# Kernel tuning notes

Measured on AMD Instinct MI355X. Metric: run time of the kernel, lower is better.

Reference implementation:

```python
import jax, jax.numpy as jnp
import numpy as np

NUM_HEADS = 16

def setup_inputs() -> dict:
    key = jax.random.key(0)
    k1, k2, k3 = jax.random.split(key, 3)
    B, S, D = 4, 2048, 1024
    x = jax.random.normal(k1, (B, S, D), dtype=jnp.float32)
    # xavier-uniform-like small init so unscaled logits stay numerically sane
    w_qkv = jax.random.normal(k2, (3 * D, D), dtype=jnp.float32) * 0.02
    w_out = jax.random.normal(k3, (D, D), dtype=jnp.float32) * 0.02
    return {"x": x, "w_qkv": w_qkv, "w_out": w_out}

def reference(x, w_qkv, w_out):
    B, S, D = x.shape
    H = NUM_HEADS
    d = D // H
    # qkv projection (Linear, no bias): x @ W^T -> [B, S, 3D]
    qkv = jnp.einsum('bsd,ed->bse', x, w_qkv).reshape(B, S, H, 3 * d)
    q, k, v = jnp.split(qkv, 3, axis=-1)           # each [B, S, H, d]
    q = q.transpose(0, 2, 1, 3)                    # [B, H, S, d]
    k = k.transpose(0, 2, 1, 3)
    v = v.transpose(0, 2, 1, 3)
    # NOTE: the original module does NOT scale by 1/sqrt(d) — faithful.
    logits = jnp.einsum('bhqd,bhkd->bhqk', q, k)   # [B, H, S, S]
    attn = jax.nn.softmax(logits, axis=-1)
    vals = jnp.einsum('bhqk,bhkd->bhqd', attn, v)  # [B, H, S, d]
    vals = vals.transpose(0, 2, 1, 3).reshape(B, S, D)
    return jnp.einsum('bsd,od->bso', vals, w_out)
```

## Files before the change

kernel.cpp:

```cpp
#include <hip/hip_runtime.h>
#include <hip/hip_bf16.h>

#define DEVINL __device__ __forceinline__

typedef short bf16x4 __attribute__((ext_vector_type(4)));
typedef short bf16x8 __attribute__((ext_vector_type(8)));
typedef float f32x4 __attribute__((ext_vector_type(4)));
typedef float f32x16 __attribute__((ext_vector_type(16)));
typedef unsigned short us4 __attribute__((ext_vector_type(4)));


DEVINL unsigned short f2bf(float f) {
  unsigned u = __builtin_bit_cast(unsigned, f);
  unsigned r = u + 0x7fffu + ((u >> 16) & 1u);
  return (unsigned short)(r >> 16);
}

DEVINL f32x4 mfma32(bf16x8 a, bf16x8 b, f32x4 c) {
  return __builtin_amdgcn_mfma_f32_16x16x32_bf16(a, b, c, 0, 0, 0);
}

DEVINL f32x16 mfma3216(bf16x8 a, bf16x8 b, f32x16 c) {
  return __builtin_amdgcn_mfma_f32_32x32x16_bf16(a, b, c, 0, 0, 0);
}

DEVINL float fexp2(float x) {
#if __has_builtin(__builtin_amdgcn_exp2f)
  return __builtin_amdgcn_exp2f(x);
#else
  return exp2f(x);
#endif
}

DEVINL unsigned cvt_pk_bf16(float a, float b) {
  unsigned r;
  asm("v_cvt_pk_bf16_f32 %0, %1, %2" : "=v"(r) : "v"(a), "v"(b));
  return r;
}

DEVINL void permswap(unsigned& x, unsigned& y) {
#if __has_builtin(__builtin_amdgcn_permlane32_swap)
  typedef int i32x2_t __attribute__((ext_vector_type(2)));
  i32x2_t r = __builtin_amdgcn_permlane32_swap((int)x, (int)y, false, false);
  x = (unsigned)r[0];
  y = (unsigned)r[1];
#else
  asm("v_permlane32_swap_b32 %0, %1" : "+v"(x), "+v"(y));
#endif
}

#define GLOAD_LDS16(g, l)                                                    \
  __builtin_amdgcn_global_load_lds(                                          \
      (__attribute__((address_space(1))) void*)(unsigned short*)(g),         \
      (__attribute__((address_space(3))) void*)(l), 16, 0, 0)

__global__ void cvtk(const float* __restrict__ src,
                     unsigned short* __restrict__ dst, int n4) {
  int i = blockIdx.x * 256 + threadIdx.x;
  const int st = gridDim.x * 256;
  for (; i < n4; i += st) {
    const float4 v = ((const float4*)src)[i];
    us4 o;
    o[0] = f2bf(v.x); o[1] = f2bf(v.y); o[2] = f2bf(v.z); o[3] = f2bf(v.w);
    ((us4*)dst)[i] = o;
  }
}

__global__ __launch_bounds__(256, 2) void qkv_gemm(
    const unsigned short* __restrict__ A,
    const unsigned short* __restrict__ Bw,
    unsigned short* __restrict__ Qo,
    unsigned short* __restrict__ Ko,
    unsigned short* __restrict__ VTo) {
  constexpr int K = 1024;
  __shared__ unsigned short SH[16384];
  const int tid = threadIdx.x;
  const int lane = tid & 63;
  const int wid = tid >> 6;
  const int l15 = lane & 15, g = lane >> 4;
  const int fid = blockIdx.y * 24 + blockIdx.x;
  const int swzid = (fid & 7) * 192 + (fid >> 3);
  const int m0 = (swzid / 24) * 128;
  const int n0 = (swzid % 24) * 128;
  const int wr = wid >> 1, wc = wid & 1;

  f32x4 acc[4][4] = {};

  const int sidx0 = tid * 8;
  const int sidx1 = (256 + tid) * 8;
  const int r0 = sidx0 >> 5, c0 = sidx0 & 31;
  const int r1 = sidx1 >> 5, c1 = sidx1 & 31;

#define QSTAGE(kt, bb)                                                       \
  {                                                                          \
    const int k0_ = (kt)*32;                                                 \
    GLOAD_LDS16(A + (size_t)(m0 + r0) * K + k0_ + c0,                        \
                SH + (bb)*8192 + sidx0);                                     \
    GLOAD_LDS16(Bw + (size_t)(n0 + r0) * K + k0_ + c0,                       \
                SH + (bb)*8192 + 4096 + sidx0);                              \
    GLOAD_LDS16(A + (size_t)(m0 + r1) * K + k0_ + c1,                        \
                SH + (bb)*8192 + sidx1);                                     \
    GLOAD_LDS16(Bw + (size_t)(n0 + r1) * K + k0_ + c1,                       \
                SH + (bb)*8192 + 4096 + sidx1);                              \
  }

  QSTAGE(0, 0);
  __syncthreads();

  for (int t = 0; t < 32; ++t) {
    const int cb = t & 1;
    if (t < 31) QSTAGE(t + 1, cb ^ 1);
    bf16x8 af[4], bfr[4];
#pragma unroll
    for (int i = 0; i < 4; ++i) {
      af[i] =
          *(const bf16x8*)(SH + cb * 8192 + (wr * 64 + i * 16 + l15) * 32 +
                           g * 8);
      bfr[i] = *(const bf16x8*)(SH + cb * 8192 + 4096 +
                                (wc * 64 + i * 16 + l15) * 32 + g * 8);
    }
#pragma unroll
    for (int mi = 0; mi < 4; ++mi)
#pragma unroll
      for (int ni = 0; ni < 4; ++ni)
        acc[mi][ni] = mfma32(af[mi], bfr[ni], acc[mi][ni]);
    __syncthreads();
  }
#undef QSTAGE

#pragma unroll
  for (int ni = 0; ni < 4; ++ni) {
    const int ebase = n0 + wc * 64 + ni * 16;
    const int h = ebase / 192;
    const int rbase = ebase - h * 192;
#pragma unroll
    for (int mi = 0; mi < 4; ++mi) {
      const int mbase = m0 + wr * 64 + mi * 16 + g * 4;
      if (rbase >= 128) {
        const int rv = rbase + l15 - 128;
        const int b = mbase >> 11, s = mbase & 2047;
        const int bh = b * 16 + h;
        us4 ov;
#pragma unroll
        for (int j = 0; j < 4; ++j) ov[j] = f2bf(acc[mi][ni][j]);
        *(us4*)(VTo + ((size_t)bh * 64 + rv) * 2048 + s) = ov;
      } else {
        const float scale = (rbase < 64) ? 1.44269504f : 1.0f;
        const int eloc = wc * 64 + ni * 16 + l15;
        const int mloc = wr * 64 + mi * 16 + g * 4;
#pragma unroll
        for (int j = 0; j < 4; ++j)
          SH[(mloc + j) * 128 + eloc] = f2bf(acc[mi][ni][j] * scale);
      }
    }
  }
  __syncthreads();
#pragma unroll
  for (int k = 0; k < 8; ++k) {
    const int c = tid + k * 256;
    const int ml = c >> 4, e8 = (c & 15) * 8;
    const int e0 = n0 + e8;
    const int h = e0 / 192;
    const int r = e0 - h * 192;
    if (r < 128) {
      const int mm = m0 + ml;
      const int b = mm >> 11, s = mm & 2047;
      const int bh = b * 16 + h;
      const bf16x8 v = *(const bf16x8*)&SH[ml * 128 + e8];
      if (r < 64)
        *(bf16x8*)(Qo + ((size_t)bh * 2048 + s) * 64 + r) = v;
      else
        *(bf16x8*)(Ko + ((size_t)bh * 2048 + s) * 64 + (r - 64)) = v;
    }
  }
}

__global__ __launch_bounds__(512, 4) void attn_fwd(
    const unsigned short* __restrict__ Q,
    const unsigned short* __restrict__ K,
    const unsigned short* __restrict__ VT,
    unsigned short* __restrict__ Vals) {
  __shared__ unsigned short Ks[2][128 * 64];
  __shared__ unsigned short Vs[2][64 * 128];
  __shared__ float invs[8][32];
  const int tid = threadIdx.x;
  const int lane = tid & 63;
  const int wid = tid >> 6;
  const int l31 = lane & 31;
  const int hi = lane >> 5;
  const int bid = (blockIdx.x & 7) * 64 + (blockIdx.x >> 3);
  const int bh = bid >> 3;
  const int q0 = (bid & 7) * 256 + wid * 32;
  const unsigned short* Qb = Q + (size_t)bh * (2048 * 64);
  const unsigned short* Kb = K + (size_t)bh * (2048 * 64);
  const unsigned short* Vb = VT + (size_t)bh * (64 * 2048);

  const unsigned short* qrow = Qb + (size_t)(q0 + l31) * 64;
  bf16x8 qf[4];
#pragma unroll
  for (int kw = 0; kw < 4; ++kw)
    qf[kw] = *(const bf16x8*)(qrow + kw * 16 + hi * 8);

  float lsum = 0.0f;
  f32x16 o0 = {}, o1 = {};
  const unsigned swz = (unsigned)((l31 & 7) << 4);
  const unsigned laneK = (unsigned)(l31 * 128) + (((unsigned)hi << 4) ^ swz);
  const unsigned laneV = (unsigned)(l31 * 256) + (((unsigned)hi << 4) ^ swz);

#define STAGE(kv0, nb)                                                       \
  {                                                                          \
    _Pragma("unroll") for (int j = 0; j < 2; ++j) {                          \
      const int c = tid + j * 512;                                           \
      const int kr = c >> 3;                                                 \
      const int ksc = ((((c & 7) << 4) ^ ((kr & 7) << 4)) >> 1);             \
      GLOAD_LDS16(Kb + (size_t)((kv0) + kr) * 64 + ksc, &Ks[nb][c * 8]);     \
      const int vr = c >> 4;                                                 \
      const int vsc = ((((c & 15) << 4) ^ ((vr & 7) << 4)) >> 1);            \
      GLOAD_LDS16(Vb + (size_t)vr * 2048 + (kv0) + vsc, &Vs[nb][c * 8]);     \
    }                                                                        \
  }

  STAGE(0, 0);
  __syncthreads();

  for (int kv0 = 0; kv0 < 2048; kv0 += 128) {
    const int cur = (kv0 >> 7) & 1;
    if (kv0 + 128 < 2048) STAGE(kv0 + 128, cur ^ 1);
    const char* kb = (const char*)Ks[cur];
    const char* vb = (const char*)Vs[cur];
#pragma unroll
    for (int sub = 0; sub < 4; ++sub) {
      const unsigned kbase = laneK + (unsigned)(sub * 4096);
      bf16x8 kf[4];
#pragma unroll
      for (int kw = 0; kw < 4; ++kw)
        kf[kw] = *(const bf16x8*)(kb + (kbase ^ (unsigned)(kw * 32)));
      f32x16 s = {};
      __builtin_amdgcn_s_setprio(1);
#pragma unroll
      for (int kw = 0; kw < 4; ++kw) s = mfma3216(kf[kw], qf[kw], s);
      __builtin_amdgcn_s_setprio(0);
#pragma unroll
      for (int half = 0; half < 2; ++half) {
        const int pb = half * 8;
        const unsigned ksoff = (unsigned)((sub * 2 + half) * 32);
        const bf16x8 vf0 = *(const bf16x8*)(vb + (laneV ^ ksoff));
        const bf16x8 vf1 = *(const bf16x8*)(vb + ((laneV + 8192u) ^ ksoff));
        const float p0 = fexp2(s[pb + 0]);
        const float p1 = fexp2(s[pb + 1]);
        const float p2 = fexp2(s[pb + 2]);
        const float p3 = fexp2(s[pb + 3]);
        const float p4 = fexp2(s[pb + 4]);
        const float p5 = fexp2(s[pb + 5]);
        const float p6 = fexp2(s[pb + 6]);
        const float p7 = fexp2(s[pb + 7]);
        lsum += ((p0 + p1) + (p2 + p3)) + ((p4 + p5) + (p6 + p7));
        unsigned w0 = cvt_pk_bf16(p0, p1);
        unsigned w2 = cvt_pk_bf16(p4, p5);
        permswap(w0, w2);
        unsigned w1 = cvt_pk_bf16(p2, p3);
        unsigned w3 = cvt_pk_bf16(p6, p7);
        permswap(w1, w3);
        union {
          unsigned u[4];
          bf16x8 v;
        } pk;
        pk.u[0] = w0;
        pk.u[1] = w1;
        pk.u[2] = w2;
        pk.u[3] = w3;
        __builtin_amdgcn_s_setprio(1);
        o0 = mfma3216(pk.v, vf0, o0);
        o1 = mfma3216(pk.v, vf1, o1);
        __builtin_amdgcn_s_setprio(0);
      }
    }
    __syncthreads();
  }
#undef STAGE

  const float ltot = lsum + __shfl_xor(lsum, 32);
  invs[wid][l31] = 1.0f / ltot;
  const int b = bh >> 4, h = bh & 15;
  unsigned short* ob = Vals + (size_t)(b * 2048 + q0) * 1024 + h * 64 + l31;
#pragma unroll
  for (int j = 0; j < 16; ++j) {
    const int ql = (j & 3) + 8 * (j >> 2) + 4 * hi;
    const float inv = invs[wid][ql];
    ob[(size_t)ql * 1024] = f2bf(o0[j] * inv);
    ob[(size_t)ql * 1024 + 32] = f2bf(o1[j] * inv);
  }
}

__global__ __launch_bounds__(256, 2) void out_gemm(
    const unsigned short* __restrict__ A,
    const unsigned short* __restrict__ Bw,
    float* __restrict__ C) {
  constexpr int K = 1024, BK = 32;
  __shared__ unsigned short As[128 * BK];
  __shared__ unsigned short Bs[128 * BK];
  const int tid = threadIdx.x;
  const int lane = tid & 63;
  const int wid = tid >> 6;
  const int l15 = lane & 15, g = lane >> 4;
  const int fid = blockIdx.y * 8 + blockIdx.x;
  const int swzid = (fid & 7) * 64 + (fid >> 3);
  const int m0 = (swzid >> 3) * 128;
  const int n0 = (swzid & 7) * 128;
  const int wr = wid >> 1, wc = wid & 1;

  f32x4 acc[4][4] = {};

  const int sidx0 = tid * 8;
  const int sidx1 = (256 + tid) * 8;
  const int r0 = sidx0 >> 5, c0 = sidx0 & 31;
  const int r1 = sidx1 >> 5, c1 = sidx1 & 31;

  for (int k0 = 0; k0 < K; k0 += BK) {
    __syncthreads();
    GLOAD_LDS16(A + (size_t)(m0 + r0) * K + k0 + c0, As + sidx0);
    GLOAD_LDS16(Bw + (size_t)(n0 + r0) * K + k0 + c0, Bs + sidx0);
    GLOAD_LDS16(A + (size_t)(m0 + r1) * K + k0 + c1, As + sidx1);
    GLOAD_LDS16(Bw + (size_t)(n0 + r1) * K + k0 + c1, Bs + sidx1);
    __syncthreads();
    bf16x8 af[4], bfr[4];
#pragma unroll
    for (int i = 0; i < 4; ++i) {
      af[i] = *(const bf16x8*)(As + (wr * 64 + i * 16 + l15) * BK + g * 8);
      bfr[i] = *(const bf16x8*)(Bs + (wc * 64 + i * 16 + l15) * BK + g * 8);
    }
#pragma unroll
    for (int mi = 0; mi < 4; ++mi)
#pragma unroll
      for (int ni = 0; ni < 4; ++ni)
        acc[mi][ni] = mfma32(af[mi], bfr[ni], acc[mi][ni]);
  }

#pragma unroll
  for (int mi = 0; mi < 4; ++mi) {
    const int mbase = m0 + wr * 64 + mi * 16 + g * 4;
#pragma unroll
    for (int ni = 0; ni < 4; ++ni) {
      const int n = n0 + wc * 64 + ni * 16 + l15;
#pragma unroll
      for (int j = 0; j < 4; ++j)
        C[(size_t)(mbase + j) * 1024 + n] = acc[mi][ni][j];
    }
  }
}

extern "C" void kernel_launch(void* const* d_in, const int* in_sizes, int n_in,
                              void* d_out, int out_size, void* d_ws,
                              size_t ws_size, hipStream_t stream) {
  const float* x = (const float*)d_in[0];
  const float* w_qkv = (const float*)d_in[1];
  const float* w_out = (const float*)d_in[2];
  float* out = (float*)d_out;

  char* ws = (char*)d_ws;
  unsigned short* xb = (unsigned short*)(ws);
  unsigned short* wqkvb = (unsigned short*)(ws + (16u << 20));
  unsigned short* woutb = (unsigned short*)(ws + (22u << 20));
  unsigned short* Qt = (unsigned short*)(ws + (24u << 20));
  unsigned short* Kt = (unsigned short*)(ws + (40u << 20));
  unsigned short* VTt = (unsigned short*)(ws + (56u << 20));
  unsigned short* vals = xb;

  cvtk<<<2048, 256, 0, stream>>>(x, xb, 8388608 / 4);
  cvtk<<<2048, 256, 0, stream>>>(w_qkv, wqkvb, 3145728 / 4);
  cvtk<<<1024, 256, 0, stream>>>(w_out, woutb, 1048576 / 4);
  qkv_gemm<<<dim3(24, 64), 256, 0, stream>>>(xb, wqkvb, Qt, Kt, VTt);
  attn_fwd<<<512, 512, 0, stream>>>(Qt, Kt, VTt, vals);
  out_gemm<<<dim3(8, 64), 256, 0, stream>>>(vals, woutb, out);
}
```

Measured before the change: 187.2 us.

## Triple-buffer GEMM LDS pipelines with vmcnt waits and fuse conversion kernels

Both projection GEMMs now use a three-stage LDS ring. Loads are issued two tiles ahead and gated by explicit s_waitcnt vmcnt plus a single s_barrier per iteration instead of two __syncthreads, and MFMA priority is raised around the compute block. The out_gemm previously had no prefetch at all. The three fp32-to-bf16 conversion launches are merged into one kernel to cut launch overhead. LDS use per block grows to 48KB, and the hand-written waitcnt accounting has to stay correct for global_load_lds.

```diff
diff --git a/kernel.cpp b/kernel.cpp
--- a/kernel.cpp
+++ b/kernel.cpp
@@ -54,15 +54,32 @@
       (__attribute__((address_space(1))) void*)(unsigned short*)(g),         \
       (__attribute__((address_space(3))) void*)(l), 16, 0, 0)
 
-__global__ void cvtk(const float* __restrict__ src,
-                     unsigned short* __restrict__ dst, int n4) {
+#define VMCNT(n) asm volatile("s_waitcnt vmcnt(" #n ")" ::: "memory")
+#define SBARRIER asm volatile("s_barrier" ::: "memory")
+
+__global__ void cvtk3(const float* __restrict__ x,
+                      const float* __restrict__ wq,
+                      const float* __restrict__ wo,
+                      unsigned short* __restrict__ xb,
+                      unsigned short* __restrict__ wqb,
+                      unsigned short* __restrict__ wob) {
   int i = blockIdx.x * 256 + threadIdx.x;
   const int st = gridDim.x * 256;
-  for (; i < n4; i += st) {
-    const float4 v = ((const float4*)src)[i];
+  for (; i < 3145728; i += st) {
+    const float* s;
+    unsigned short* d;
+    int j = i;
+    if (j < 2097152) {
+      s = x; d = xb;
+    } else if (j < 2097152 + 786432) {
+      j -= 2097152; s = wq; d = wqb;
+    } else {
+      j -= 2097152 + 786432; s = wo; d = wob;
+    }
+    const float4 v = ((const float4*)s)[j];
     us4 o;
     o[0] = f2bf(v.x); o[1] = f2bf(v.y); o[2] = f2bf(v.z); o[3] = f2bf(v.w);
-    ((us4*)dst)[i] = o;
+    ((us4*)d)[j] = o;
   }
 }
 
@@ -73,7 +90,7 @@
     unsigned short* __restrict__ Ko,
     unsigned short* __restrict__ VTo) {
   constexpr int K = 1024;
-  __shared__ unsigned short SH[16384];
+  __shared__ unsigned short SH[24576];
   const int tid = threadIdx.x;
   const int lane = tid & 63;
   const int wid = tid >> 6;
@@ -105,28 +122,38 @@
   }
 
   QSTAGE(0, 0);
-  __syncthreads();
+  QSTAGE(1, 1);
+  VMCNT(4);
+  SBARRIER;
 
   for (int t = 0; t < 32; ++t) {
-    const int cb = t & 1;
-    if (t < 31) QSTAGE(t + 1, cb ^ 1);
+    const int cb = t - (t / 3) * 3;
+    const unsigned short* bufA = SH + cb * 8192;
+    const unsigned short* bufB = bufA + 4096;
     bf16x8 af[4], bfr[4];
 #pragma unroll
     for (int i = 0; i < 4; ++i) {
-      af[i] =
-          *(const bf16x8*)(SH + cb * 8192 + (wr * 64 + i * 16 + l15) * 32 +
-                           g * 8);
-      bfr[i] = *(const bf16x8*)(SH + cb * 8192 + 4096 +
-                                (wc * 64 + i * 16 + l15) * 32 + g * 8);
-    }
+      af[i] = *(const bf16x8*)(bufA + (wr * 64 + i * 16 + l15) * 32 + g * 8);
+      bfr[i] = *(const bf16x8*)(bufB + (wc * 64 + i * 16 + l15) * 32 + g * 8);
+    }
+    if (t < 30) {
+      const int nb = (t + 2) - ((t + 2) / 3) * 3;
+      QSTAGE(t + 2, nb);
+      VMCNT(4);
+    } else if (t == 30) {
+      VMCNT(0);
+    }
+    SBARRIER;
+    __builtin_amdgcn_s_setprio(1);
 #pragma unroll
     for (int mi = 0; mi < 4; ++mi)
 #pragma unroll
       for (int ni = 0; ni < 4; ++ni)
         acc[mi][ni] = mfma32(af[mi], bfr[ni], acc[mi][ni]);
-    __syncthreads();
+    __builtin_amdgcn_s_setprio(0);
   }
 #undef QSTAGE
+  __syncthreads();
 
 #pragma unroll
   for (int ni = 0; ni < 4; ++ni) {
@@ -296,9 +323,8 @@
     const unsigned short* __restrict__ A,
     const unsigned short* __restrict__ Bw,
     float* __restrict__ C) {
-  constexpr int K = 1024, BK = 32;
-  __shared__ unsigned short As[128 * BK];
-  __shared__ unsigned short Bs[128 * BK];
+  constexpr int K = 1024;
+  __shared__ unsigned short SH[24576];
   const int tid = threadIdx.x;
   const int lane = tid & 63;
   const int wid = tid >> 6;
@@ -316,25 +342,51 @@
   const int r0 = sidx0 >> 5, c0 = sidx0 & 31;
   const int r1 = sidx1 >> 5, c1 = sidx1 & 31;
 
-  for (int k0 = 0; k0 < K; k0 += BK) {
-    __syncthreads();
-    GLOAD_LDS16(A + (size_t)(m0 + r0) * K + k0 + c0, As + sidx0);
-    GLOAD_LDS16(Bw + (size_t)(n0 + r0) * K + k0 + c0, Bs + sidx0);
-    GLOAD_LDS16(A + (size_t)(m0 + r1) * K + k0 + c1, As + sidx1);
-    GLOAD_LDS16(Bw + (size_t)(n0 + r1) * K + k0 + c1, Bs + sidx1);
-    __syncthreads();
+#define OSTAGE(kt, bb)                                                       \
+  {                                                                          \
+    const int k0_ = (kt)*32;                                                 \
+    GLOAD_LDS16(A + (size_t)(m0 + r0) * K + k0_ + c0,                        \
+                SH + (bb)*8192 + sidx0);                                     \
+    GLOAD_LDS16(Bw + (size_t)(n0 + r0) * K + k0_ + c0,                       \
+                SH + (bb)*8192 + 4096 + sidx0);                              \
+    GLOAD_LDS16(A + (size_t)(m0 + r1) * K + k0_ + c1,                        \
+                SH + (bb)*8192 + sidx1);                                     \
+    GLOAD_LDS16(Bw + (size_t)(n0 + r1) * K + k0_ + c1,                       \
+                SH + (bb)*8192 + 4096 + sidx1);                              \
+  }
+
+  OSTAGE(0, 0);
+  OSTAGE(1, 1);
+  VMCNT(4);
+  SBARRIER;
+
+  for (int t = 0; t < 32; ++t) {
+    const int cb = t - (t / 3) * 3;
+    const unsigned short* bufA = SH + cb * 8192;
+    const unsigned short* bufB = bufA + 4096;
     bf16x8 af[4], bfr[4];
 #pragma unroll
     for (int i = 0; i < 4; ++i) {
-      af[i] = *(const bf16x8*)(As + (wr * 64 + i * 16 + l15) * BK + g * 8);
-      bfr[i] = *(const bf16x8*)(Bs + (wc * 64 + i * 16 + l15) * BK + g * 8);
-    }
+      af[i] = *(const bf16x8*)(bufA + (wr * 64 + i * 16 + l15) * 32 + g * 8);
+      bfr[i] = *(const bf16x8*)(bufB + (wc * 64 + i * 16 + l15) * 32 + g * 8);
+    }
+    if (t < 30) {
+      const int nb = (t + 2) - ((t + 2) / 3) * 3;
+      OSTAGE(t + 2, nb);
+      VMCNT(4);
+    } else if (t == 30) {
+      VMCNT(0);
+    }
+    SBARRIER;
+    __builtin_amdgcn_s_setprio(1);
 #pragma unroll
     for (int mi = 0; mi < 4; ++mi)
 #pragma unroll
       for (int ni = 0; ni < 4; ++ni)
         acc[mi][ni] = mfma32(af[mi], bfr[ni], acc[mi][ni]);
-  }
+    __builtin_amdgcn_s_setprio(0);
+  }
+#undef OSTAGE
 
 #pragma unroll
   for (int mi = 0; mi < 4; ++mi) {
@@ -366,9 +418,7 @@
   unsigned short* VTt = (unsigned short*)(ws + (56u << 20));
   unsigned short* vals = xb;
 
-  cvtk<<<2048, 256, 0, stream>>>(x, xb, 8388608 / 4);
-  cvtk<<<2048, 256, 0, stream>>>(w_qkv, wqkvb, 3145728 / 4);
-  cvtk<<<1024, 256, 0, stream>>>(w_out, woutb, 1048576 / 4);
+  cvtk3<<<2048, 256, 0, stream>>>(x, w_qkv, w_out, xb, wqkvb, woutb);
   qkv_gemm<<<dim3(24, 64), 256, 0, stream>>>(xb, wqkvb, Qt, Kt, VTt);
   attn_fwd<<<512, 512, 0, stream>>>(Qt, Kt, VTt, vals);
   out_gemm<<<dim3(8, 64), 256, 0, stream>>>(vals, woutb, out);
```

Result: faster. 179.0 us, median of 2 (-4.4%).
